# Optimization experiments

Measured on AMD Instinct MI355X. Metric: run time of the kernel, lower is better.

## Reference

```python
import jax, jax.numpy as jnp
import numpy as np

EPS = 1e-6      # vn_layers EPS
BN_EPS = 1e-5   # torch BatchNorm eps
NEG = 0.2       # LeakyReLU negative slope
K = 20


def setup_inputs() -> dict:
    key = jax.random.key(0)
    ks = jax.random.split(key, 10)
    B, C, N = 4, 384, 2048
    return {
        'x': jax.random.normal(ks[0], (B, C, N), jnp.float32),
        'w_kc1_feat': jax.random.normal(ks[1], (21, 256), jnp.float32) * 0.05,
        'w_kc1_dir': jax.random.normal(ks[2], (21, 256), jnp.float32) * 0.05,
        'w_kc2_feat': jax.random.normal(ks[3], (21, 21), jnp.float32) * 0.05,
        'w_kc2_dir': jax.random.normal(ks[4], (21, 21), jnp.float32) * 0.05,
        'w_pool_dir': jax.random.normal(ks[5], (21, 21), jnp.float32) * 0.05,
        'w_conv1': jax.random.normal(ks[6], (256, 63), jnp.float32) * 0.05,
        'w_conv2': jax.random.normal(ks[7], (128, 256), jnp.float32) * 0.05,
        'w_conv3': jax.random.normal(ks[8], (1, 128), jnp.float32) * 0.05,
        'b_conv3': jnp.zeros((1,), jnp.float32),
    }


def knn_idx(xf, k):
    # xf: (B, C, N) -> (B, N, k) indices of k nearest neighbors (neg sq dist top-k)
    inner = -2.0 * jnp.einsum('bcn,bcm->bnm', xf, xf)
    xx = jnp.sum(xf * xf, axis=1)  # (B, N)
    neg_dist = -(xx[:, :, None] + inner + xx[:, None, :])
    _, idx = jax.lax.top_k(neg_dist, k)
    return idx


def get_graph_feature(x, k):
    # x: (B, C3, 3, N) -> (B, 2*C3, 3, N, k)
    B, C3, _, N = x.shape
    xf = x.reshape(B, C3 * 3, N)
    idx = knn_idx(xf, k)                      # (B, N, k)
    xt = jnp.transpose(xf, (0, 2, 1))         # (B, N, C3*3)
    feat = jax.vmap(lambda a, i: a[i])(xt, idx)  # (B, N, k, C3*3)
    feat = feat.reshape(B, N, k, C3, 3)
    xc = xt.reshape(B, N, 1, C3, 3)
    out = jnp.concatenate([feat - xc, jnp.broadcast_to(xc, feat.shape)], axis=3)
    return jnp.transpose(out, (0, 3, 4, 1, 2))  # (B, 2C3, 3, N, k)


def vn_bn(x):
    # VNBatchNorm (dim=5), training-mode batch stats, no affine (gamma=1, beta=0)
    norm = jnp.linalg.norm(x, axis=2) + EPS          # (B, C, N, K)
    mean = jnp.mean(norm, axis=(0, 2, 3), keepdims=True)
    var = jnp.mean((norm - mean) ** 2, axis=(0, 2, 3), keepdims=True)
    norm_bn = (norm - mean) / jnp.sqrt(var + BN_EPS)
    return x / norm[:, :, None] * norm_bn[:, :, None]


def vn_block(x, w_feat, w_dir):
    # VNLinearLeakyReLU: x (B, Cin, 3, N, K)
    p = jnp.einsum('oc,bcvnk->bovnk', w_feat, x)
    p = vn_bn(p)
    d = jnp.einsum('oc,bcvnk->bovnk', w_dir, x)
    dot = jnp.sum(p * d, axis=2, keepdims=True)
    d2 = jnp.sum(d * d, axis=2, keepdims=True)
    proj = p - (dot / (d2 + EPS)) * d
    return NEG * p + (1.0 - NEG) * jnp.where(dot >= 0, p, proj)


def vn_max_pool(x, w_dir):
    # x: (B, C, 3, N, K) -> (B, C, 3, N)
    d = jnp.einsum('oc,bcvnk->bovnk', w_dir, x)
    dot = jnp.sum(x * d, axis=2, keepdims=True)        # (B, C, 1, N, K)
    idx = jnp.argmax(dot, axis=-1)                     # (B, C, 1, N)
    idx = jnp.broadcast_to(idx[..., None], x.shape[:-1] + (1,))
    return jnp.take_along_axis(x, idx, axis=-1)[..., 0]


def conv_bn_lrelu(x, w):
    # 1x1 Conv1d (no bias) + BatchNorm1d (batch stats) + LeakyReLU(0.2)
    y = jnp.einsum('oc,bcn->bon', w, x)
    mean = jnp.mean(y, axis=(0, 2), keepdims=True)
    var = jnp.mean((y - mean) ** 2, axis=(0, 2), keepdims=True)
    y = (y - mean) / jnp.sqrt(var + BN_EPS)
    return jnp.where(y >= 0, y, NEG * y)


def reference(x, w_kc1_feat, w_kc1_dir, w_kc2_feat, w_kc2_dir, w_pool_dir,
              w_conv1, w_conv2, w_conv3, b_conv3):
    B, C, N = x.shape
    h = x[:, None]                      # (B, 1, in_dim, N) -> treated as (B, C3, 3, N)
    h = h.reshape(B, C // 3, 3, N)
    h = get_graph_feature(h, K)         # (B, 2*C//3, 3, N, K)
    h = vn_block(h, w_kc1_feat, w_kc1_dir)
    h = vn_block(h, w_kc2_feat, w_kc2_dir)
    h = vn_max_pool(h, w_pool_dir)      # (B, 21, 3, N)
    h = h.reshape(B, 63, N)
    h = conv_bn_lrelu(h, w_conv1)
    h = conv_bn_lrelu(h, w_conv2)
    # dropout is identity (inference); final 1x1 conv with bias
    out = jnp.einsum('oc,bcn->bon', w_conv3, h) + b_conv3[None, :, None]
    return out[:, 0, :]                 # squeeze(dim=-2) -> (B, N)
```

## Files before the change

### kernel.cpp

```cpp
#include <hip/hip_runtime.h>
#include <cstddef>

#define BB 4
#define CC 384
#define NPT 2048
#define KNN 20
#define NCAND 32
#define NCH 21
#define NKT (NPT*KNN)
#define TOT (BB*NKT)
#define EPSD 1e-6
#define BNEPSD 1e-5
#define EPSF 1e-6f
#define BNEPS 1e-5f
#define NEGS 0.2f

__global__ __launch_bounds__(256) void k_zero(float* p, int n) {
    int t = blockIdx.x*256 + threadIdx.x;
    if (t < n) p[t] = 0.f;
}

__global__ __launch_bounds__(256) void k_xx(const float* __restrict__ x, float* __restrict__ xx,
                                            double* __restrict__ xxd) {
    int t = blockIdx.x*256 + threadIdx.x;
    int n = t & (NPT-1); int b = t >> 11;
    const float* xp = x + (size_t)b*CC*NPT + n;
    double acc = 0.0;
    #pragma unroll 8
    for (int c = 0; c < CC; c++) { double v = (double)xp[(size_t)c*NPT]; acc += v*v; }
    xx[t] = (float)acc;
    xxd[t] = acc;
}

__global__ __launch_bounds__(256) void k_xt(const float* __restrict__ x, float* __restrict__ xT) {
    __shared__ float tile[64][65];
    int n0 = blockIdx.x*64, c0 = blockIdx.y*64, b = blockIdx.z;
    int tx = threadIdx.x & 63, ty = threadIdx.x >> 6;
    const float* xb = x + (size_t)b*CC*NPT;
    #pragma unroll
    for (int r = 0; r < 64; r += 4)
        tile[r+ty][tx] = xb[(size_t)(c0+r+ty)*NPT + n0 + tx];
    __syncthreads();
    float* xtb = xT + (size_t)b*NPT*CC;
    #pragma unroll
    for (int r = 0; r < 64; r += 4)
        xtb[(size_t)(n0+r+ty)*CC + c0 + tx] = tile[tx][r+ty];
}

__global__ __launch_bounds__(256) void k_gram(const float* __restrict__ x, const float* __restrict__ xx,
                                              float* __restrict__ scores4) {
    __shared__ float As[16][128];
    __shared__ float Bs[16][128];
    int tid = blockIdx.x;
    int b = blockIdx.y;
    int by = 0, rem = tid;
    while (rem >= 16 - by) { rem -= 16 - by; by++; }
    int bx = by + rem;
    int n0 = by*128, m0 = bx*128;
    int t = threadIdx.x;
    int tx = t & 15, ty = t >> 4;
    const float* xb = x + (size_t)b*CC*NPT;
    float* scores = scores4 + (size_t)b*NPT*NPT;
    float acc[8][8] = {};
    for (int c0 = 0; c0 < CC; c0 += 16) {
        #pragma unroll
        for (int i = 0; i < 8; i++) {
            int e = t + i*256;
            int cc = e >> 7, col = e & 127;
            As[cc][col] = xb[(size_t)(c0+cc)*NPT + n0 + col];
            Bs[cc][col] = xb[(size_t)(c0+cc)*NPT + m0 + col];
        }
        __syncthreads();
        #pragma unroll
        for (int kk = 0; kk < 16; kk++) {
            float4 a0 = *(const float4*)&As[kk][ty*8];
            float4 a1 = *(const float4*)&As[kk][ty*8+4];
            float4 b0 = *(const float4*)&Bs[kk][tx*8];
            float4 b1 = *(const float4*)&Bs[kk][tx*8+4];
            float av[8] = {a0.x,a0.y,a0.z,a0.w,a1.x,a1.y,a1.z,a1.w};
            float bv[8] = {b0.x,b0.y,b0.z,b0.w,b1.x,b1.y,b1.z,b1.w};
            #pragma unroll
            for (int i = 0; i < 8; i++)
                #pragma unroll
                for (int j = 0; j < 8; j++)
                    acc[i][j] += av[i]*bv[j];
        }
        __syncthreads();
    }
    int nb = n0 + ty*8, mb = m0 + tx*8;
    float xn[8], xm[8];
    #pragma unroll
    for (int i = 0; i < 8; i++) { xn[i] = xx[b*NPT + nb + i]; xm[i] = xx[b*NPT + mb + i]; }
    float val[8][8];
    #pragma unroll
    for (int i = 0; i < 8; i++)
        #pragma unroll
        for (int j = 0; j < 8; j++) {
            val[i][j] = 2.f*acc[i][j] - xn[i] - xm[j];
            scores[(size_t)(nb+i)*NPT + mb + j] = val[i][j];
        }
    if (bx != by) {
        #pragma unroll
        for (int j = 0; j < 8; j++)
            #pragma unroll
            for (int i = 0; i < 8; i++)
                scores[(size_t)(mb+j)*NPT + nb + i] = val[i][j];
    }
}

__global__ __launch_bounds__(256) void k_topk(const float* __restrict__ scores4, int* __restrict__ candout) {
    int n = blockIdx.x, b = blockIdx.y;
    const float* row = scores4 + ((size_t)b*NPT + n)*NPT;
    unsigned key[8];
    #pragma unroll
    for (int w = 0; w < 8; w++) {
        unsigned u = __float_as_uint(row[threadIdx.x + w*256]);
        key[w] = (u & 0x80000000u) ? ~u : (u | 0x80000000u);
    }
    __shared__ int hist[4][257];
    __shared__ int histsum[256];
    __shared__ unsigned s_pfx;
    __shared__ int s_need, s_slot, s_tie;
    __shared__ unsigned long long tiel[256];
    int wv = threadIdx.x >> 6;
    if (threadIdx.x == 0) { s_pfx = 0u; s_need = NCAND; s_slot = 0; s_tie = 0; }
    #pragma unroll
    for (int pass = 0; pass < 3; pass++) {
        int sh = (pass == 0) ? 24 : (pass == 1 ? 16 : 8);
        unsigned maskhi = (pass == 0) ? 0u : (pass == 1 ? 0xFF000000u : 0xFFFF0000u);
        hist[0][threadIdx.x] = 0; hist[1][threadIdx.x] = 0;
        hist[2][threadIdx.x] = 0; hist[3][threadIdx.x] = 0;
        __syncthreads();
        unsigned pfx = s_pfx;
        #pragma unroll
        for (int w = 0; w < 8; w++) {
            unsigned v = key[w];
            if ((v & maskhi) == (pfx & maskhi))
                atomicAdd(&hist[wv][(v >> sh) & 0xFF], 1);
        }
        __syncthreads();
        histsum[threadIdx.x] = hist[0][threadIdx.x] + hist[1][threadIdx.x]
                             + hist[2][threadIdx.x] + hist[3][threadIdx.x];
        __syncthreads();
        if (threadIdx.x < 64) {
            int l = threadIdx.x, base = l*4;
            int c0 = histsum[base], c1 = histsum[base+1], c2 = histsum[base+2], c3 = histsum[base+3];
            int mysum = c0 + c1 + c2 + c3;
            int suf = mysum;
            #pragma unroll
            for (int st = 1; st < 64; st <<= 1) {
                int u2 = __shfl_down(suf, st);
                if (l + st >= 64) u2 = 0;
                suf += u2;
            }
            int need = s_need;
            int sufNext = suf - mysum;
            if (suf >= need && sufNext < need) {
                int s3 = sufNext + c3, s2p = s3 + c2, s1p = s2p + c1;
                int B, Sb1;
                if (s3 >= need)       { B = base+3; Sb1 = sufNext; }
                else if (s2p >= need) { B = base+2; Sb1 = s3; }
                else if (s1p >= need) { B = base+1; Sb1 = s2p; }
                else                  { B = base;   Sb1 = s1p; }
                s_pfx = s_pfx | ((unsigned)B << sh);
                s_need = need - Sb1;
            }
        }
        __syncthreads();
    }
    unsigned pfx24 = s_pfx & 0xFFFFFF00u;
    int* outp = candout + ((size_t)b*NPT + n)*NCAND;
    #pragma unroll
    for (int w = 0; w < 8; w++) {
        unsigned v = key[w];
        unsigned hi = v & 0xFFFFFF00u;
        int i = threadIdx.x + w*256;
        if (hi > pfx24) {
            int s = atomicAdd(&s_slot, 1);
            outp[s] = i;
        } else if (hi == pfx24) {
            int ti = atomicAdd(&s_tie, 1);
            if (ti < 256) tiel[ti] = ((unsigned long long)v << 32) | (unsigned)(NPT-1-i);
        }
    }
    __syncthreads();
    if (threadIdx.x == 0) {
        int A = s_slot, r = s_need, T = s_tie < 256 ? s_tie : 256;
        for (int kk = 0; kk < r; kk++) {
            unsigned long long best = 0ull; int bj = 0;
            for (int j2 = 0; j2 < T; j2++) if (tiel[j2] > best) { best = tiel[j2]; bj = j2; }
            tiel[bj] = 0ull;
            outp[A + kk] = NPT-1-(int)(best & 0xFFFFFFFFu);
        }
    }
}

__global__ __launch_bounds__(256) void k_rescore(const float* __restrict__ xT, const double* __restrict__ xxd,
                                                 const int* __restrict__ cand, int* __restrict__ idxout) {
    __shared__ float xn[CC];
    __shared__ double sc[NCAND];
    __shared__ int ci[NCAND];
    int t = blockIdx.x;
    int b = t >> 11;
    const float* xrow = xT + (size_t)t*CC;
    for (int i = threadIdx.x; i < CC; i += 256) xn[i] = xrow[i];
    if (threadIdx.x < NCAND) ci[threadIdx.x] = cand[(size_t)t*NCAND + threadIdx.x];
    __syncthreads();
    int j = threadIdx.x >> 3, l = threadIdx.x & 7;
    int m = ci[j];
    const float* xm = xT + ((size_t)b*NPT + m)*CC;
    double acc = 0.0;
    int cbase = l*48;
    #pragma unroll 8
    for (int c = 0; c < 48; c++) acc += (double)xn[cbase+c] * (double)xm[cbase+c];
    acc += __shfl_down(acc, 4, 8);
    acc += __shfl_down(acc, 2, 8);
    acc += __shfl_down(acc, 1, 8);
    if (l == 0) sc[j] = 2.0*acc - xxd[t] - xxd[(size_t)b*NPT + m];
    __syncthreads();
    if (threadIdx.x < 64) {
        double v = (threadIdx.x < NCAND) ? sc[threadIdx.x] : -1e300;
        int oi = (threadIdx.x < NCAND) ? ci[threadIdx.x] : NPT;
        for (int kk = 0; kk < KNN; kk++) {
            double bv = v; int bo = oi;
            #pragma unroll
            for (int st = 16; st > 0; st >>= 1) {
                double ov = __shfl_xor(bv, st, 32);
                int    oo = __shfl_xor(bo, st, 32);
                if (ov > bv || (ov == bv && oo < bo)) { bv = ov; bo = oo; }
            }
            if (threadIdx.x == 0) idxout[(size_t)t*KNN + kk] = bo;
            if (oi == bo) v = -1e300;
        }
    }
}

__global__ __launch_bounds__(256) void k_pq_d(const float* __restrict__ xT,
                                              const float* __restrict__ wf, const float* __restrict__ wd,
                                              double* __restrict__ Pf, double* __restrict__ Qf,
                                              double* __restrict__ Pd, double* __restrict__ Qd) {
    __shared__ float xs[4][CC];
    __shared__ float wfa[128*NCH];
    __shared__ float wfb[128*NCH];
    __shared__ float wda[128*NCH];
    __shared__ float wdb[128*NCH];
    int pt = threadIdx.x >> 6;
    int ov = threadIdx.x & 63;
    int row0 = blockIdx.x*4;
    for (int i = threadIdx.x; i < 4*CC; i += 256)
        xs[i/CC][i%CC] = xT[(size_t)(row0 + i/CC)*CC + (i%CC)];
    for (int i = threadIdx.x; i < 128*NCH; i += 256) {
        int o2 = i >> 7, c3 = i & 127;
        wfa[c3*NCH+o2] = wf[o2*256 + c3];
        wfb[c3*NCH+o2] = wf[o2*256 + 128 + c3];
        wda[c3*NCH+o2] = wd[o2*256 + c3];
        wdb[c3*NCH+o2] = wd[o2*256 + 128 + c3];
    }
    __syncthreads();
    if (ov >= 63) return;
    int o = ov / 3, v = ov % 3;
    const float* xp = &xs[pt][v];
    double pf = 0.0, qf = 0.0, pd = 0.0, qd = 0.0;
    #pragma unroll 4
    for (int c3 = 0; c3 < 128; c3++) {
        double xv = (double)xp[c3*3];
        double waf = (double)wfa[c3*NCH+o], wbf = (double)wfb[c3*NCH+o];
        double wad = (double)wda[c3*NCH+o], wbd = (double)wdb[c3*NCH+o];
        pf += waf*xv; qf += (wbf-waf)*xv;
        pd += wad*xv; qd += (wbd-wad)*xv;
    }
    size_t off = (size_t)(row0 + pt)*64 + ov;
    Pf[off] = pf; Qf[off] = qf; Pd[off] = pd; Qd[off] = qd;
}

__global__ __launch_bounds__(256) void k_bn1_part(const double* __restrict__ Pf, const double* __restrict__ Qf,
                                                  const int* __restrict__ idx, double* __restrict__ part) {
    __shared__ double red[4][42];
    int t = blockIdx.x*256 + threadIdx.x;
    int bn = t / KNN;
    int n = bn & (NPT-1); int b = bn >> 11;
    int m = idx[t];
    const double* PF = Pf + ((size_t)b*NPT + m)*64;
    const double* QF = Qf + ((size_t)b*NPT + n)*64;
    int wave = threadIdx.x >> 6;
    #pragma unroll
    for (int o = 0; o < NCH; o++) {
        double p0 = PF[o*3+0] + QF[o*3+0];
        double p1 = PF[o*3+1] + QF[o*3+1];
        double p2 = PF[o*3+2] + QF[o*3+2];
        double nr = sqrt(p0*p0 + p1*p1 + p2*p2) + EPSD;
        double a = nr, c2 = nr*nr;
        #pragma unroll
        for (int st = 32; st > 0; st >>= 1) { a += __shfl_down(a, st); c2 += __shfl_down(c2, st); }
        if ((threadIdx.x & 63) == 0) { red[wave][o] = a; red[wave][NCH+o] = c2; }
    }
    __syncthreads();
    if (threadIdx.x < 42)
        part[(size_t)blockIdx.x*42 + threadIdx.x] =
            red[0][threadIdx.x] + red[1][threadIdx.x] + red[2][threadIdx.x] + red[3][threadIdx.x];
}

__global__ __launch_bounds__(256) void k_fin_d(const double* __restrict__ part, double* __restrict__ st,
                                               int nblk, double cnt) {
    __shared__ double r0[4], r1[4];
    int o = blockIdx.x;
    double s0 = 0.0, s1 = 0.0;
    for (int i = threadIdx.x; i < nblk; i += 256) {
        s0 += part[(size_t)i*42 + o];
        s1 += part[(size_t)i*42 + NCH + o];
    }
    #pragma unroll
    for (int stp = 32; stp > 0; stp >>= 1) { s0 += __shfl_down(s0, stp); s1 += __shfl_down(s1, stp); }
    int wv = threadIdx.x >> 6;
    if ((threadIdx.x & 63) == 0) { r0[wv] = s0; r1[wv] = s1; }
    __syncthreads();
    if (threadIdx.x == 0) {
        double sum = r0[0]+r0[1]+r0[2]+r0[3];
        double ssq = r1[0]+r1[1]+r1[2]+r1[3];
        double mean = sum / cnt;
        double var = ssq / cnt - mean*mean;
        if (var < 0.0) var = 0.0;
        st[o] = mean;
        st[NCH+o] = 1.0 / sqrt(var + BNEPSD);
    }
}

__global__ __launch_bounds__(256) void k_b1_bn2part(const double* __restrict__ Pf, const double* __restrict__ Qf,
                                                    const double* __restrict__ Pd, const double* __restrict__ Qd,
                                                    const int* __restrict__ idx, const double* __restrict__ st1,
                                                    const float* __restrict__ w2f_g, double* __restrict__ part) {
    __shared__ double h1L[32][65];
    __shared__ double w2s[NCH*NCH];
    __shared__ double s1[42];
    __shared__ double wred[4][42];
    int tid = threadIdx.x;
    int p = tid >> 3, j = tid & 7;
    int t = blockIdx.x*32 + p;
    for (int i = tid; i < NCH*NCH; i += 256) w2s[i] = (double)w2f_g[i];
    if (tid < 42) s1[tid] = st1[tid];
    int bn = t / KNN;
    int n = bn & (NPT-1), b = bn >> 11;
    int m = idx[t];
    const double* PF = Pf + ((size_t)b*NPT + m)*64;
    const double* QF = Qf + ((size_t)b*NPT + n)*64;
    const double* PD = Pd + ((size_t)b*NPT + m)*64;
    const double* QD = Qd + ((size_t)b*NPT + n)*64;
    __syncthreads();
    for (int o = j; o < NCH; o += 8) {
        double p0 = PF[o*3+0] + QF[o*3+0];
        double p1 = PF[o*3+1] + QF[o*3+1];
        double p2 = PF[o*3+2] + QF[o*3+2];
        double d0 = PD[o*3+0] + QD[o*3+0];
        double d1 = PD[o*3+1] + QD[o*3+1];
        double d2 = PD[o*3+2] + QD[o*3+2];
        double nr = sqrt(p0*p0 + p1*p1 + p2*p2) + EPSD;
        double fac = (nr - s1[o]) * s1[NCH+o] / nr;
        p0 *= fac; p1 *= fac; p2 *= fac;
        double dot = p0*d0 + p1*d1 + p2*d2;
        double dd  = d0*d0 + d1*d1 + d2*d2;
        double coef = dot / (dd + EPSD);
        double w0 = (dot >= 0.0) ? p0 : (p0 - coef*d0);
        double w1 = (dot >= 0.0) ? p1 : (p1 - coef*d1);
        double w2 = (dot >= 0.0) ? p2 : (p2 - coef*d2);
        h1L[p][o*3+0] = 0.2*p0 + 0.8*w0;
        h1L[p][o*3+1] = 0.2*p1 + 0.8*w1;
        h1L[p][o*3+2] = 0.2*p2 + 0.8*w2;
    }
    __syncthreads();
    double s[3] = {0.0,0.0,0.0}, q[3] = {0.0,0.0,0.0};
    {
        int oi = 0;
        for (int o = j; o < NCH; o += 8, oi++) {
            double a0 = 0.0, a1 = 0.0, a2 = 0.0;
            #pragma unroll
            for (int c = 0; c < NCH; c++) {
                double w = w2s[o*NCH+c];
                a0 += w*h1L[p][c*3+0]; a1 += w*h1L[p][c*3+1]; a2 += w*h1L[p][c*3+2];
            }
            double nr = sqrt(a0*a0 + a1*a1 + a2*a2) + EPSD;
            s[oi] = nr; q[oi] = nr*nr;
        }
    }
    #pragma unroll
    for (int st = 8; st < 64; st <<= 1) {
        #pragma unroll
        for (int u = 0; u < 3; u++) { s[u] += __shfl_down(s[u], st); q[u] += __shfl_down(q[u], st); }
    }
    if ((tid & 63) < 8) {
        int wv = tid >> 6, oi = 0;
        for (int o = j; o < NCH; o += 8, oi++) { wred[wv][o] = s[oi]; wred[wv][NCH+o] = q[oi]; }
    }
    __syncthreads();
    if (tid < 42)
        part[(size_t)blockIdx.x*42 + tid] = wred[0][tid]+wred[1][tid]+wred[2][tid]+wred[3][tid];
}

__global__ __launch_bounds__(256) void k_apply_d(const double* __restrict__ Pf, const double* __restrict__ Qf,
                                                 const double* __restrict__ Pd, const double* __restrict__ Qd,
                                                 const int* __restrict__ idx,
                                                 const double* __restrict__ st1, const double* __restrict__ st2,
                                                 const float* __restrict__ w2f_g, const float* __restrict__ w2d_g,
                                                 const float* __restrict__ wp_g,
                                                 float* __restrict__ h2f, double* __restrict__ dots) {
    __shared__ double hL[32][65];
    __shared__ double w2fs[NCH*NCH];
    __shared__ double w2ds[NCH*NCH];
    __shared__ double wps[NCH*NCH];
    __shared__ double s1[42], s2[42];
    int tid = threadIdx.x;
    int p = tid >> 3, j = tid & 7;
    int t = blockIdx.x*32 + p;
    for (int i = tid; i < NCH*NCH; i += 256) {
        w2fs[i] = (double)w2f_g[i]; w2ds[i] = (double)w2d_g[i]; wps[i] = (double)wp_g[i];
    }
    if (tid < 42) { s1[tid] = st1[tid]; s2[tid] = st2[tid]; }
    int k = t % KNN; int bn = t / KNN;
    int n = bn & (NPT-1), b = bn >> 11;
    int m = idx[t];
    const double* PF = Pf + ((size_t)b*NPT + m)*64;
    const double* QF = Qf + ((size_t)b*NPT + n)*64;
    const double* PD = Pd + ((size_t)b*NPT + m)*64;
    const double* QD = Qd + ((size_t)b*NPT + n)*64;
    __syncthreads();
    #pragma unroll
    for (int oi = 0; oi < 3; oi++) {
        int o = j + oi*8;
        if (o < NCH) {
            double p0 = PF[o*3+0] + QF[o*3+0];
            double p1 = PF[o*3+1] + QF[o*3+1];
            double p2 = PF[o*3+2] + QF[o*3+2];
            double d0 = PD[o*3+0] + QD[o*3+0];
            double d1 = PD[o*3+1] + QD[o*3+1];
            double d2 = PD[o*3+2] + QD[o*3+2];
            double nr = sqrt(p0*p0 + p1*p1 + p2*p2) + EPSD;
            double fac = (nr - s1[o]) * s1[NCH+o] / nr;
            p0 *= fac; p1 *= fac; p2 *= fac;
            double dot = p0*d0 + p1*d1 + p2*d2;
            double dd  = d0*d0 + d1*d1 + d2*d2;
            double coef = dot / (dd + EPSD);
            double w0 = (dot >= 0.0) ? p0 : (p0 - coef*d0);
            double w1 = (dot >= 0.0) ? p1 : (p1 - coef*d1);
            double w2 = (dot >= 0.0) ? p2 : (p2 - coef*d2);
            hL[p][o*3+0] = 0.2*p0 + 0.8*w0;
            hL[p][o*3+1] = 0.2*p1 + 0.8*w1;
            hL[p][o*3+2] = 0.2*p2 + 0.8*w2;
        }
    }
    __syncthreads();
    double h2r[3][3];
    #pragma unroll
    for (int oi = 0; oi < 3; oi++) {
        int o = j + oi*8;
        if (o < NCH) {
            double p0 = 0.0, p1 = 0.0, p2 = 0.0, d0 = 0.0, d1 = 0.0, d2 = 0.0;
            #pragma unroll
            for (int c = 0; c < NCH; c++) {
                double wa = w2fs[o*NCH+c], wb = w2ds[o*NCH+c];
                double x0 = hL[p][c*3+0], x1 = hL[p][c*3+1], x2 = hL[p][c*3+2];
                p0 += wa*x0; p1 += wa*x1; p2 += wa*x2;
                d0 += wb*x0; d1 += wb*x1; d2 += wb*x2;
            }
            double nr = sqrt(p0*p0 + p1*p1 + p2*p2) + EPSD;
            double fac = (nr - s2[o]) * s2[NCH+o] / nr;
            p0 *= fac; p1 *= fac; p2 *= fac;
            double dot = p0*d0 + p1*d1 + p2*d2;
            double dd  = d0*d0 + d1*d1 + d2*d2;
            double coef = dot / (dd + EPSD);
            double w0 = (dot >= 0.0) ? p0 : (p0 - coef*d0);
            double w1 = (dot >= 0.0) ? p1 : (p1 - coef*d1);
            double w2 = (dot >= 0.0) ? p2 : (p2 - coef*d2);
            double h0 = 0.2*p0 + 0.8*w0, h1v = 0.2*p1 + 0.8*w1, h2v = 0.2*p2 + 0.8*w2;
            h2r[oi][0] = h0; h2r[oi][1] = h1v; h2r[oi][2] = h2v;
            h2f[((size_t)(b*63 + o*3+0)*NPT + n)*KNN + k] = (float)h0;
            h2f[((size_t)(b*63 + o*3+1)*NPT + n)*KNN + k] = (float)h1v;
            h2f[((size_t)(b*63 + o*3+2)*NPT + n)*KNN + k] = (float)h2v;
        }
    }
    __syncthreads();
    #pragma unroll
    for (int oi = 0; oi < 3; oi++) {
        int o = j + oi*8;
        if (o < NCH) {
            hL[p][o*3+0] = h2r[oi][0];
            hL[p][o*3+1] = h2r[oi][1];
            hL[p][o*3+2] = h2r[oi][2];
        }
    }
    __syncthreads();
    #pragma unroll
    for (int oi = 0; oi < 3; oi++) {
        int o = j + oi*8;
        if (o < NCH) {
            double dv0 = 0.0, dv1 = 0.0, dv2 = 0.0;
            #pragma unroll
            for (int c = 0; c < NCH; c++) {
                double w = wps[o*NCH+c];
                dv0 += w*hL[p][c*3+0]; dv1 += w*hL[p][c*3+1]; dv2 += w*hL[p][c*3+2];
            }
            double dt = hL[p][o*3+0]*dv0 + hL[p][o*3+1]*dv1 + hL[p][o*3+2]*dv2;
            dots[(((size_t)b*NCH + o)*NPT + n)*KNN + k] = dt;
        }
    }
}

__global__ __launch_bounds__(32) void k_pool_d(const double* __restrict__ dots, const float* __restrict__ h2f,
                                               float* __restrict__ pooled) {
    int b = blockIdx.x >> 11, n = blockIdx.x & (NPT-1);
    int o = threadIdx.x;
    if (o >= NCH) return;
    const double* dp = dots + (((size_t)b*NCH + o)*NPT + n)*KNN;
    double best = dp[0]; int bk = 0;
    #pragma unroll
    for (int k = 1; k < KNN; k++) { double v = dp[k]; if (v > best) { best = v; bk = k; } }
    #pragma unroll
    for (int v = 0; v < 3; v++)
        pooled[((size_t)b*63 + o*3+v)*NPT + n] = h2f[(((size_t)b*63 + o*3+v)*NPT + n)*KNN + bk];
}

__global__ __launch_bounds__(256) void k_conv1(const float* __restrict__ pooled, const float* __restrict__ w1,
                                               float* __restrict__ y1, float* __restrict__ sums) {
    int n = blockIdx.x*256 + threadIdx.x;
    int o = blockIdx.y, b = blockIdx.z;
    const float* pb = pooled + (size_t)b*63*NPT + n;
    const float* wo = w1 + o*63;
    float acc = 0.f;
    #pragma unroll
    for (int c = 0; c < 63; c++) acc += wo[c]*pb[(size_t)c*NPT];
    y1[((size_t)b*256 + o)*NPT + n] = acc;
    float a = acc, c2 = acc*acc;
    #pragma unroll
    for (int st = 32; st > 0; st >>= 1) { a += __shfl_down(a, st); c2 += __shfl_down(c2, st); }
    __shared__ float ra[4], rc[4];
    int wv = threadIdx.x >> 6;
    if ((threadIdx.x & 63) == 0) { ra[wv] = a; rc[wv] = c2; }
    __syncthreads();
    if (threadIdx.x == 0) {
        atomicAdd(&sums[o], ra[0]+ra[1]+ra[2]+ra[3]);
        atomicAdd(&sums[256+o], rc[0]+rc[1]+rc[2]+rc[3]);
    }
}

__global__ void k_finalize(const float* __restrict__ sums, float* __restrict__ stats, float invcnt, int nch) {
    int o = blockIdx.x*blockDim.x + threadIdx.x;
    if (o >= nch) return;
    float mean = sums[o]*invcnt;
    float var = sums[nch+o]*invcnt - mean*mean;
    if (var < 0.f) var = 0.f;
    stats[o] = mean;
    stats[nch+o] = 1.0f / sqrtf(var + BNEPS);
}

__global__ __launch_bounds__(256) void k_act(float* __restrict__ y, const float* __restrict__ stats, int nch) {
    int t = blockIdx.x*256 + threadIdx.x;
    int o = (t >> 11) % nch;
    float z = (y[t] - stats[o]) * stats[nch+o];
    y[t] = z >= 0.f ? z : NEGS*z;
}

__global__ __launch_bounds__(256) void k_conv2(const float* __restrict__ z1, const float* __restrict__ w2,
                                               float* __restrict__ y2, float* __restrict__ sums) {
    int n = blockIdx.x*256 + threadIdx.x;
    int o = blockIdx.y, b = blockIdx.z;
    const float* pb = z1 + (size_t)b*256*NPT + n;
    const float* wo = w2 + o*256;
    float acc = 0.f;
    #pragma unroll 4
    for (int c = 0; c < 256; c++) acc += wo[c]*pb[(size_t)c*NPT];
    y2[((size_t)b*128 + o)*NPT + n] = acc;
    float a = acc, c2 = acc*acc;
    #pragma unroll
    for (int st = 32; st > 0; st >>= 1) { a += __shfl_down(a, st); c2 += __shfl_down(c2, st); }
    __shared__ float ra[4], rc[4];
    int wv = threadIdx.x >> 6;
    if ((threadIdx.x & 63) == 0) { ra[wv] = a; rc[wv] = c2; }
    __syncthreads();
    if (threadIdx.x == 0) {
        atomicAdd(&sums[o], ra[0]+ra[1]+ra[2]+ra[3]);
        atomicAdd(&sums[128+o], rc[0]+rc[1]+rc[2]+rc[3]);
    }
}

__global__ __launch_bounds__(256) void k_final(const float* __restrict__ y2, const float* __restrict__ w3,
                                               const float* __restrict__ b3, const float* __restrict__ stats,
                                               float* __restrict__ out) {
    int t = blockIdx.x*256 + threadIdx.x;
    int n = t & (NPT-1); int b = t >> 11;
    const float* yb = y2 + (size_t)b*128*NPT + n;
    float acc = b3[0];
    #pragma unroll 4
    for (int c = 0; c < 128; c++) {
        float z = (yb[(size_t)c*NPT] - stats[c]) * stats[128+c];
        z = z >= 0.f ? z : NEGS*z;
        acc += w3[c]*z;
    }
    out[t] = acc;
}

extern "C" void kernel_launch(void* const* d_in, const int* in_sizes, int n_in,
                              void* d_out, int out_size, void* d_ws, size_t ws_size,
                              hipStream_t stream) {
    const float* x   = (const float*)d_in[0];
    const float* w1f = (const float*)d_in[1];
    const float* w1d = (const float*)d_in[2];
    const float* w2f = (const float*)d_in[3];
    const float* w2d = (const float*)d_in[4];
    const float* wp  = (const float*)d_in[5];
    const float* wc1 = (const float*)d_in[6];
    const float* wc2 = (const float*)d_in[7];
    const float* wc3 = (const float*)d_in[8];
    const float* bc3 = (const float*)d_in[9];
    float* out = (float*)d_out;

    float* ws = (float*)d_ws;
    float*  scores4 = ws;
    float*  xxf     = ws + 16777216;
    double* xxd     = (double*)(ws + 16785408);
    int*    cand    = (int*)(ws + 16801792);
    int*    idx     = (int*)(ws + 17063936);
    float*  xT      = ws + 17227776;
    double* Pfd     = (double*)(ws + 20373504);
    double* Qfd     = (double*)(ws + 21422080);
    double* Pdd     = (double*)(ws + 22470656);
    double* Qdd     = (double*)(ws + 23519232);
    double* part1   = (double*)(ws + 24567808);
    double* part2   = (double*)(ws + 24621568);
    double* st1     = (double*)(ws + 25051648);
    double* st2     = (double*)(ws + 25051776);
    float*  sums_f  = ws + 25051904;
    float*  stats_f = ws + 25052928;
    double* dots    = (double*)(ws + 25053952);
    float*  h2f     = ws + 31935232;
    float*  pooled  = ws + 42257152;
    float*  y1      = ws + 42773248;
    float*  y2      = ws + 44870400;

    k_zero<<<4, 256, 0, stream>>>(sums_f, 1024);
    k_xx<<<BB*NPT/256, 256, 0, stream>>>(x, xxf, xxd);
    k_xt<<<dim3(NPT/64, CC/64, BB), 256, 0, stream>>>(x, xT);
    k_gram<<<dim3(136, BB), 256, 0, stream>>>(x, xxf, scores4);
    k_topk<<<dim3(NPT, BB), 256, 0, stream>>>(scores4, cand);
    k_rescore<<<BB*NPT, 256, 0, stream>>>(xT, xxd, cand, idx);
    k_pq_d<<<BB*NPT/4, 256, 0, stream>>>(xT, w1f, w1d, Pfd, Qfd, Pdd, Qdd);
    k_bn1_part<<<TOT/256, 256, 0, stream>>>(Pfd, Qfd, idx, part1);
    k_fin_d<<<NCH, 256, 0, stream>>>(part1, st1, TOT/256, (double)TOT);
    k_b1_bn2part<<<TOT/32, 256, 0, stream>>>(Pfd, Qfd, Pdd, Qdd, idx, st1, w2f, part2);
    k_fin_d<<<NCH, 256, 0, stream>>>(part2, st2, TOT/32, (double)TOT);
    k_apply_d<<<TOT/32, 256, 0, stream>>>(Pfd, Qfd, Pdd, Qdd, idx, st1, st2, w2f, w2d, wp, h2f, dots);
    k_pool_d<<<BB*NPT, 32, 0, stream>>>(dots, h2f, pooled);
    k_conv1<<<dim3(NPT/256, 256, BB), 256, 0, stream>>>(pooled, wc1, y1, sums_f);
    k_finalize<<<1, 256, 0, stream>>>(sums_f, stats_f, 1.f/(float)(BB*NPT), 256);
    k_act<<<BB*256*NPT/256, 256, 0, stream>>>(y1, stats_f, 256);
    k_conv2<<<dim3(NPT/256, 128, BB), 256, 0, stream>>>(y1, wc2, y2, sums_f+512);
    k_finalize<<<1, 128, 0, stream>>>(sums_f+512, stats_f+512, 1.f/(float)(BB*NPT), 128);
    k_final<<<BB*NPT/256, 256, 0, stream>>>(y2, wc3, bc3, stats_f+512, out);
}
```

Before: 666.8 us.

## Shrink gram tiles to 64x64 and compute norms from transposed rows

The Gram-matrix kernel moves from 128x128 tiles with 8x8 per-thread accumulators to 64x64 tiles with 4x4 accumulators. This raises the block count from 136 to 528 per batch, improving occupancy and load balance on the many-CU GPU, but halves arithmetic intensity per shared-memory load. The squared-norm kernel now runs after the transpose and reads contiguous xT rows with one wavefront per point and a shuffle reduction. This replaces a strided per-thread column walk over 384 channels.

```diff
diff --git a/kernel.cpp b/kernel.cpp
--- a/kernel.cpp
+++ b/kernel.cpp
@@ -20,18 +20,6 @@
     if (t < n) p[t] = 0.f;
 }
 
-__global__ __launch_bounds__(256) void k_xx(const float* __restrict__ x, float* __restrict__ xx,
-                                            double* __restrict__ xxd) {
-    int t = blockIdx.x*256 + threadIdx.x;
-    int n = t & (NPT-1); int b = t >> 11;
-    const float* xp = x + (size_t)b*CC*NPT + n;
-    double acc = 0.0;
-    #pragma unroll 8
-    for (int c = 0; c < CC; c++) { double v = (double)xp[(size_t)c*NPT]; acc += v*v; }
-    xx[t] = (float)acc;
-    xxd[t] = acc;
-}
-
 __global__ __launch_bounds__(256) void k_xt(const float* __restrict__ x, float* __restrict__ xT) {
     __shared__ float tile[64][65];
     int n0 = blockIdx.x*64, c0 = blockIdx.y*64, b = blockIdx.z;
@@ -47,63 +35,71 @@
         xtb[(size_t)(n0+r+ty)*CC + c0 + tx] = tile[tx][r+ty];
 }
 
+__global__ __launch_bounds__(256) void k_xx(const float* __restrict__ xT, float* __restrict__ xx,
+                                            double* __restrict__ xxd) {
+    int pid = blockIdx.x*4 + (threadIdx.x >> 6);
+    int lane = threadIdx.x & 63;
+    const float* row = xT + (size_t)pid*CC;
+    double acc = 0.0;
+    #pragma unroll
+    for (int c = lane; c < CC; c += 64) { double v = (double)row[c]; acc += v*v; }
+    #pragma unroll
+    for (int st = 32; st > 0; st >>= 1) acc += __shfl_down(acc, st);
+    if (lane == 0) { xx[pid] = (float)acc; xxd[pid] = acc; }
+}
+
 __global__ __launch_bounds__(256) void k_gram(const float* __restrict__ x, const float* __restrict__ xx,
                                               float* __restrict__ scores4) {
-    __shared__ float As[16][128];
-    __shared__ float Bs[16][128];
+    __shared__ float As[16][64];
+    __shared__ float Bs[16][64];
     int tid = blockIdx.x;
     int b = blockIdx.y;
     int by = 0, rem = tid;
-    while (rem >= 16 - by) { rem -= 16 - by; by++; }
+    while (rem >= 32 - by) { rem -= 32 - by; by++; }
     int bx = by + rem;
-    int n0 = by*128, m0 = bx*128;
+    int n0 = by*64, m0 = bx*64;
     int t = threadIdx.x;
     int tx = t & 15, ty = t >> 4;
     const float* xb = x + (size_t)b*CC*NPT;
     float* scores = scores4 + (size_t)b*NPT*NPT;
-    float acc[8][8] = {};
+    float acc[4][4] = {};
     for (int c0 = 0; c0 < CC; c0 += 16) {
         #pragma unroll
-        for (int i = 0; i < 8; i++) {
+        for (int i = 0; i < 4; i++) {
             int e = t + i*256;
-            int cc = e >> 7, col = e & 127;
+            int cc = e >> 6, col = e & 63;
             As[cc][col] = xb[(size_t)(c0+cc)*NPT + n0 + col];
             Bs[cc][col] = xb[(size_t)(c0+cc)*NPT + m0 + col];
         }
         __syncthreads();
         #pragma unroll
         for (int kk = 0; kk < 16; kk++) {
-            float4 a0 = *(const float4*)&As[kk][ty*8];
-            float4 a1 = *(const float4*)&As[kk][ty*8+4];
-            float4 b0 = *(const float4*)&Bs[kk][tx*8];
-            float4 b1 = *(const float4*)&Bs[kk][tx*8+4];
-            float av[8] = {a0.x,a0.y,a0.z,a0.w,a1.x,a1.y,a1.z,a1.w};
-            float bv[8] = {b0.x,b0.y,b0.z,b0.w,b1.x,b1.y,b1.z,b1.w};
-            #pragma unroll
-            for (int i = 0; i < 8; i++)
-                #pragma unroll
-                for (int j = 0; j < 8; j++)
-                    acc[i][j] += av[i]*bv[j];
+            float4 a  = *(const float4*)&As[kk][ty*4];
+            float4 bv = *(const float4*)&Bs[kk][tx*4];
+            acc[0][0] += a.x*bv.x; acc[0][1] += a.x*bv.y; acc[0][2] += a.x*bv.z; acc[0][3] += a.x*bv.w;
+            acc[1][0] += a.y*bv.x; acc[1][1] += a.y*bv.y; acc[1][2] += a.y*bv.z; acc[1][3] += a.y*bv.w;
+            acc[2][0] += a.z*bv.x; acc[2][1] += a.z*bv.y; acc[2][2] += a.z*bv.z; acc[2][3] += a.z*bv.w;
+            acc[3][0] += a.w*bv.x; acc[3][1] += a.w*bv.y; acc[3][2] += a.w*bv.z; acc[3][3] += a.w*bv.w;
         }
         __syncthreads();
     }
-    int nb = n0 + ty*8, mb = m0 + tx*8;
-    float xn[8], xm[8];
-    #pragma unroll
-    for (int i = 0; i < 8; i++) { xn[i] = xx[b*NPT + nb + i]; xm[i] = xx[b*NPT + mb + i]; }
-    float val[8][8];
-    #pragma unroll
-    for (int i = 0; i < 8; i++)
+    int nb = n0 + ty*4, mb = m0 + tx*4;
+    float xn[4], xm[4];
+    #pragma unroll
+    for (int i = 0; i < 4; i++) { xn[i] = xx[b*NPT + nb + i]; xm[i] = xx[b*NPT + mb + i]; }
+    float val[4][4];
+    #pragma unroll
+    for (int i = 0; i < 4; i++)
         #pragma unroll
-        for (int j = 0; j < 8; j++) {
+        for (int j = 0; j < 4; j++) {
             val[i][j] = 2.f*acc[i][j] - xn[i] - xm[j];
             scores[(size_t)(nb+i)*NPT + mb + j] = val[i][j];
         }
     if (bx != by) {
         #pragma unroll
-        for (int j = 0; j < 8; j++)
+        for (int j = 0; j < 4; j++)
             #pragma unroll
-            for (int i = 0; i < 8; i++)
+            for (int i = 0; i < 4; i++)
                 scores[(size_t)(mb+j)*NPT + nb + i] = val[i][j];
     }
 }
@@ -635,9 +631,9 @@
     float*  y2      = ws + 44870400;
 
     k_zero<<<4, 256, 0, stream>>>(sums_f, 1024);
-    k_xx<<<BB*NPT/256, 256, 0, stream>>>(x, xxf, xxd);
     k_xt<<<dim3(NPT/64, CC/64, BB), 256, 0, stream>>>(x, xT);
-    k_gram<<<dim3(136, BB), 256, 0, stream>>>(x, xxf, scores4);
+    k_xx<<<BB*NPT/4, 256, 0, stream>>>(xT, xxf, xxd);
+    k_gram<<<dim3(528, BB), 256, 0, stream>>>(x, xxf, scores4);
     k_topk<<<dim3(NPT, BB), 256, 0, stream>>>(scores4, cand);
     k_rescore<<<BB*NPT, 256, 0, stream>>>(xT, xxd, cand, idx);
     k_pq_d<<<BB*NPT/4, 256, 0, stream>>>(xT, w1f, w1d, Pfd, Qfd, Pdd, Qdd);
```

Result: faster. 629.4 us (-5.6%).
